# Kernel tuning notes

Measured on AMD Instinct MI355X. Metric: run time of the kernel, lower is better.

The kernel has to match this reference:

```python
import jax, jax.numpy as jnp
import numpy as np

N0, N1, N2 = 120000, 40000, 10000   # sampled node counts per hop
E0, E1 = 600000, 150000             # edges per block (fanout ~15)
DIN, DH, NC = 128, 256, 47


def _glorot(k, fan_in, fan_out):
    s = (2.0 / (fan_in + fan_out)) ** 0.5
    return jax.random.normal(k, (fan_in, fan_out), jnp.float32) * s


def setup_inputs() -> dict:
    key = jax.random.key(0)
    ks = jax.random.split(key, 20)
    x0 = jax.random.normal(ks[0], (N0, DIN), jnp.float32)
    src0 = jax.random.randint(ks[1], (E0,), 0, N0)
    dst0 = jax.random.randint(ks[2], (E0,), 0, N1)
    src1 = jax.random.randint(ks[3], (E1,), 0, N1)
    dst1 = jax.random.randint(ks[4], (E1,), 0, N2)
    srcb0 = jax.random.randint(ks[5], (E0,), 0, N0)
    dstb0 = jax.random.randint(ks[6], (E0,), 0, N1)
    srcb1 = jax.random.randint(ks[7], (E1,), 0, N1)
    dstb1 = jax.random.randint(ks[8], (E1,), 0, N2)
    # id_old_value_new: must satisfy idx[:n] < n for every truncation length n,
    # i.e. idx[k] in [0, k+1)
    rng = np.random.default_rng(0)
    idx = jnp.asarray((rng.random(N0) * (np.arange(N0) + 1)).astype(np.int64))
    mix_ratio = jnp.float32(0.5)
    Wl0 = _glorot(ks[9], DIN, DH); Wr0 = _glorot(ks[10], DIN, DH)
    b0 = jnp.zeros((DH,), jnp.float32)
    Wl1 = _glorot(ks[11], DH, DH); Wr1 = _glorot(ks[12], DH, DH)
    b1 = jnp.zeros((DH,), jnp.float32)
    Wlin = _glorot(ks[13], DH, NC)
    blin = jnp.zeros((NC,), jnp.float32)
    return dict(x0=x0, src0=src0, dst0=dst0, src1=src1, dst1=dst1,
                srcb0=srcb0, dstb0=dstb0, srcb1=srcb1, dstb1=dstb1,
                idx=idx, mix_ratio=mix_ratio,
                Wl0=Wl0, Wr0=Wr0, b0=b0, Wl1=Wl1, Wr1=Wr1, b1=b1,
                Wlin=Wlin, blin=blin)


def _sage(x_all, root_x, src, dst, n_root, Wl, Wr, b):
    # PyG-style SAGEConv, mean aggregation: lin_l(mean_j x_j) + lin_r(root)
    msgs = x_all[src]                                        # [E, D] gather
    s = jax.ops.segment_sum(msgs, dst, num_segments=n_root)  # [n_root, D]
    cnt = jax.ops.segment_sum(jnp.ones_like(dst, dtype=x_all.dtype), dst,
                              num_segments=n_root)
    mean = s / jnp.maximum(cnt, 1.0)[:, None]
    return mean @ Wl + root_x @ Wr + b


def reference(x0, src0, dst0, src1, dst1, srcb0, dstb0, srcb1, dstb1,
              idx, mix_ratio, Wl0, Wr0, b0, Wl1, Wr1, b1, Wlin, blin):
    blocks = [(src0, dst0, N1), (src1, dst1, N2)]
    blocks_b = [(srcb0, dstb0, N1), (srcb1, dstb1, N2)]
    params = [(Wl0, Wr0, b0), (Wl1, Wr1, b1)]
    m = mix_ratio

    # first branch (dropout omitted: inference mode)
    aggr_xs = [x0]
    for i in range(2):
        src, dst, n_root = blocks[i]
        Wl, Wr, b = params[i]
        root_x = aggr_xs[-1][:n_root]
        x = jax.nn.relu(_sage(aggr_xs[-1], root_x, src, dst, n_root, Wl, Wr, b))
        aggr_xs.append(x)

    # permuted branch via id_old_value_new gather
    aggr_xs_b = [x[idx[: x.shape[0]]] for x in aggr_xs]

    x_mix = aggr_xs[0] * m + aggr_xs_b[0] * (1.0 - m)
    for i in range(2):
        src, dst, n_root = blocks[i]
        srcb, dstb, n_root_b = blocks_b[i]
        Wl, Wr, b = params[i]
        x_new = jax.nn.relu(_sage(aggr_xs[i], x_mix[:n_root], src, dst,
                                  n_root, Wl, Wr, b))
        x_new_b = jax.nn.relu(_sage(aggr_xs_b[i], x_mix[:n_root_b], srcb, dstb,
                                    n_root_b, Wl, Wr, b))
        x_mix = x_new * m + x_new_b * (1.0 - m)

    logits = x_mix @ Wlin + blin
    return jax.nn.log_softmax(logits, axis=-1)
```

## Files before the change

### kernel.cpp

```cpp
#include <hip/hip_runtime.h>
#include <math.h>

#define N1C 40000
#define N2C 10000
#define DIN 128
#define DH  256
#define NC  47

#define TOTCNT (2 * N1C + 2 * N2C)
#define CAP 64
#define CURSTR 16

typedef __attribute__((ext_vector_type(8))) short v8s;
typedef __attribute__((ext_vector_type(4))) float v4f;
typedef __attribute__((ext_vector_type(2))) float v2f;

#if __has_builtin(__builtin_amdgcn_cvt_pk_f32_fp8)
#define HW_FP8 1
#endif

__device__ __forceinline__ unsigned short f2bf(float f) {
    unsigned int u = __float_as_uint(f);
    u += 0x7FFF + ((u >> 16) & 1);
    return (unsigned short)(u >> 16);
}
__device__ __forceinline__ float bf2f(unsigned int h) {
    return __uint_as_float(h << 16);
}

__device__ __forceinline__ unsigned char f2e4m3(float f) {
    unsigned int u = __float_as_uint(f);
    unsigned char s = (unsigned char)((u >> 24) & 0x80);
    float a = __uint_as_float(u & 0x7FFFFFFF);
    if (a > 448.0f) a = 448.0f;
    if (a < 0.015625f) {
        int k = (int)rintf(a * 512.0f);
        return s | (unsigned char)k;
    }
    unsigned int bits = __float_as_uint(a);
    int et = (int)(bits >> 23) - 127 + 7;
    unsigned int m32 = bits & 0x7FFFFF;
    unsigned int m3 = m32 >> 20;
    unsigned int rest = m32 & 0xFFFFF;
    if (rest > 0x80000 || (rest == 0x80000 && (m3 & 1))) m3++;
    if (m3 == 8) { m3 = 0; et++; }
    if (et > 15 || (et == 15 && m3 == 7)) return s | 0x7E;
    return s | (unsigned char)((et << 3) | m3);
}

__device__ __forceinline__ void dec4(unsigned int u, float& f0, float& f1,
                                     float& f2, float& f3) {
#ifdef HW_FP8
    v2f lo = __builtin_amdgcn_cvt_pk_f32_fp8((int)u, false);
    v2f hi = __builtin_amdgcn_cvt_pk_f32_fp8((int)u, true);
    f0 = lo[0]; f1 = lo[1]; f2 = hi[0]; f3 = hi[1];
#else
    auto d1 = [](unsigned int b) -> float {
        int e = (b >> 3) & 15, mm = b & 7;
        float d = (e == 0) ? (float)mm * (1.0f / 512.0f)
                           : (1.0f + (float)mm * 0.125f) * exp2f((float)(e - 7));
        return (b & 0x80) ? -d : d;
    };
    f0 = d1(u & 0xFF); f1 = d1((u >> 8) & 0xFF);
    f2 = d1((u >> 16) & 0xFF); f3 = d1(u >> 24);
#endif
}

__global__ __launch_bounds__(256) void front_fused(
        const int* __restrict__ src0, const int* __restrict__ dst0,
        const int* __restrict__ srcb0, const int* __restrict__ dstb0,
        const int* __restrict__ src1, const int* __restrict__ dst1,
        const int* __restrict__ srcb1, const int* __restrict__ dstb1,
        const int* __restrict__ perm, int* __restrict__ cur,
        int* __restrict__ bucket, int E0, int E1, int nbFill,
        const float* __restrict__ x0, unsigned char* __restrict__ x0f,
        long n8, int nbConv,
        const float* __restrict__ Wl0, const float* __restrict__ Wr0,
        const float* __restrict__ Wl1, const float* __restrict__ Wr1,
        unsigned short* __restrict__ Wt0l, unsigned short* __restrict__ Wt0r,
        unsigned short* __restrict__ Wt1l, unsigned short* __restrict__ Wt1r) {
    int b = blockIdx.x, t = threadIdx.x;
    if (b < nbFill) {
        int e = b * 256 + t;
        int tot = 2 * E0 + 2 * E1;
        if (e >= tot) return;
        int s, bin;
        if (e < E0) {
            s = src0[e];                  bin = dst0[e];
        } else if (e < 2 * E0) {
            int le = e - E0;
            s = perm[srcb0[le]];          bin = N1C + dstb0[le];
        } else if (e < 2 * E0 + E1) {
            int le = e - 2 * E0;
            s = src1[le];                 bin = 2 * N1C + dst1[le];
        } else {
            int le = e - 2 * E0 - E1;
            s = perm[srcb1[le]];          bin = 2 * N1C + N2C + dstb1[le];
        }
        int pos = atomicAdd(&cur[(size_t)bin * CURSTR], 1);
        if (pos < CAP) bucket[(size_t)bin * CAP + pos] = s;
    } else if (b < nbFill + nbConv) {
        long i = (long)(b - nbFill) * 256 + t;
        if (i >= n8) return;
        const float4* p = (const float4*)(x0 + i * 8);
        float4 a = p[0], c = p[1];
        float f[8] = {a.x, a.y, a.z, a.w, c.x, c.y, c.z, c.w};
        unsigned int q0 = 0, q1 = 0;
#pragma unroll
        for (int j = 0; j < 8; j++) {
            unsigned int e8 = f2e4m3(f[j]);
            if (j < 4) q0 |= e8 << (8 * j); else q1 |= e8 << (8 * (j - 4));
        }
        uint2 q = {q0, q1};
        *(uint2*)(x0f + i * 8) = q;
    } else {
        int id = (b - nbFill - nbConv) * 256 + t;
        const int S0 = DIN * DH;
        const int S1 = DH * DH;
        const float* W; unsigned short* Wt; int K, loc;
        if (id < S0)                   { W = Wl0; Wt = Wt0l; K = DIN; loc = id; }
        else if (id < 2 * S0)          { W = Wr0; Wt = Wt0r; K = DIN; loc = id - S0; }
        else if (id < 2 * S0 + S1)     { W = Wl1; Wt = Wt1l; K = DH;  loc = id - 2 * S0; }
        else if (id < 2 * S0 + 2 * S1) { W = Wr1; Wt = Wt1r; K = DH;  loc = id - 2 * S0 - S1; }
        else return;
        int n = loc / K, k = loc - n * K;
        Wt[(size_t)n * K + k] = f2bf(W[(size_t)k * DH + n]);
    }
}

__global__ __launch_bounds__(256) void gather_mean_128f(
        const unsigned char* __restrict__ xf, const int* __restrict__ bucket,
        const int* __restrict__ cur, unsigned short* __restrict__ mean0,
        unsigned short* __restrict__ meanb0) {
    const int half = N1C / 8;
    int b = blockIdx.x;
    int binbase; unsigned short* outp; int rb;
    if (b < half) { binbase = 0;   outp = mean0;  rb = b; }
    else          { binbase = N1C; outp = meanb0; rb = b - half; }
    int wv = threadIdx.x >> 6, lane = threadIdx.x & 63;
    int row = rb * 8 + wv * 2 + (lane >> 5);
    int c4 = (lane & 31) * 4;
    int bin = binbase + row;
    int cnt = min(cur[(size_t)bin * CURSTR], CAP);
    const int* cs = bucket + (size_t)bin * CAP;
    float a0 = 0.0f, a1 = 0.0f, a2 = 0.0f, a3 = 0.0f;
    int i = 0;
    for (; i + 3 < cnt; i += 4) {
        int s0 = cs[i], s1 = cs[i + 1], s2 = cs[i + 2], s3 = cs[i + 3];
        unsigned int u = *(const unsigned int*)&xf[(size_t)s0 * DIN + c4];
        unsigned int v = *(const unsigned int*)&xf[(size_t)s1 * DIN + c4];
        unsigned int w = *(const unsigned int*)&xf[(size_t)s2 * DIN + c4];
        unsigned int z = *(const unsigned int*)&xf[(size_t)s3 * DIN + c4];
        float u0, u1, u2, u3, w0, w1, w2, w3, p0, p1, p2, p3, q0, q1, q2, q3;
        dec4(u, u0, u1, u2, u3);
        dec4(v, w0, w1, w2, w3);
        dec4(w, p0, p1, p2, p3);
        dec4(z, q0, q1, q2, q3);
        a0 += (u0 + w0) + (p0 + q0); a1 += (u1 + w1) + (p1 + q1);
        a2 += (u2 + w2) + (p2 + q2); a3 += (u3 + w3) + (p3 + q3);
    }
    for (; i < cnt; i++) {
        unsigned int u = *(const unsigned int*)&xf[(size_t)cs[i] * DIN + c4];
        float u0, u1, u2, u3;
        dec4(u, u0, u1, u2, u3);
        a0 += u0; a1 += u1; a2 += u2; a3 += u3;
    }
    float inv = 1.0f / (float)max(cnt, 1);
    uint2 o;
    o.x = (unsigned int)f2bf(a0 * inv) | ((unsigned int)f2bf(a1 * inv) << 16);
    o.y = (unsigned int)f2bf(a2 * inv) | ((unsigned int)f2bf(a3 * inv) << 16);
    *(uint2*)&outp[(size_t)row * DIN + c4] = o;
}

__global__ __launch_bounds__(256) void gather_mean_256f(
        const unsigned char* __restrict__ xf, const int* __restrict__ bucket,
        const int* __restrict__ cur, unsigned short* __restrict__ mean1,
        unsigned short* __restrict__ meanb1) {
    const int half = N2C / 4;
    int b = blockIdx.x;
    int binbase; unsigned short* outp; int rb;
    if (b < half) { binbase = 2 * N1C;       outp = mean1;  rb = b; }
    else          { binbase = 2 * N1C + N2C; outp = meanb1; rb = b - half; }
    int row = rb * 4 + (threadIdx.x >> 6);
    int lane = threadIdx.x & 63;
    int bin = binbase + row;
    int cnt = min(cur[(size_t)bin * CURSTR], CAP);
    const int* cs = bucket + (size_t)bin * CAP;
    float a0 = 0.0f, a1 = 0.0f, a2 = 0.0f, a3 = 0.0f;
    int i = 0;
    for (; i + 3 < cnt; i += 4) {
        int s0 = cs[i], s1 = cs[i + 1], s2 = cs[i + 2], s3 = cs[i + 3];
        unsigned int u = *(const unsigned int*)&xf[(size_t)s0 * DH + lane * 4];
        unsigned int v = *(const unsigned int*)&xf[(size_t)s1 * DH + lane * 4];
        unsigned int w = *(const unsigned int*)&xf[(size_t)s2 * DH + lane * 4];
        unsigned int z = *(const unsigned int*)&xf[(size_t)s3 * DH + lane * 4];
        float u0, u1, u2, u3, w0, w1, w2, w3, p0, p1, p2, p3, q0, q1, q2, q3;
        dec4(u, u0, u1, u2, u3);
        dec4(v, w0, w1, w2, w3);
        dec4(w, p0, p1, p2, p3);
        dec4(z, q0, q1, q2, q3);
        a0 += (u0 + w0) + (p0 + q0); a1 += (u1 + w1) + (p1 + q1);
        a2 += (u2 + w2) + (p2 + q2); a3 += (u3 + w3) + (p3 + q3);
    }
    for (; i < cnt; i++) {
        unsigned int u = *(const unsigned int*)&xf[(size_t)cs[i] * DH + lane * 4];
        float u0, u1, u2, u3;
        dec4(u, u0, u1, u2, u3);
        a0 += u0; a1 += u1; a2 += u2; a3 += u3;
    }
    float inv = 1.0f / (float)max(cnt, 1);
    uint2 o;
    o.x = (unsigned int)f2bf(a0 * inv) | ((unsigned int)f2bf(a1 * inv) << 16);
    o.y = (unsigned int)f2bf(a2 * inv) | ((unsigned int)f2bf(a3 * inv) << 16);
    *(uint2*)&outp[(size_t)row * DH + lane * 4] = o;
}

#define KP0 136
#define H0T 5
__global__ __launch_bounds__(256, 2) void hop0_mfma(
        const float* __restrict__ x0, const int* __restrict__ idx,
        const unsigned short* __restrict__ mean0, const unsigned short* __restrict__ meanb0,
        const unsigned short* __restrict__ Wtl, const unsigned short* __restrict__ Wtr,
        const float* __restrict__ b, const float* __restrict__ mixp,
        unsigned char* __restrict__ x1f, unsigned short* __restrict__ xm1) {
    __shared__ unsigned short Alds[4][16][KP0];
    int t = threadIdx.x;
    int wv = t >> 6, lane = t & 63;
    int mrow = lane & 15, quad = lane >> 4;
    float m = *mixp;

    v8s wl[4][4], wr[4][4];
    float bb[4];
#pragma unroll
    for (int ct = 0; ct < 4; ct++) {
        int n = wv * 64 + mrow * 4 + ct;
        bb[ct] = b[n];
#pragma unroll
        for (int ks = 0; ks < 4; ks++) {
            int k0 = ks * 32 + quad * 8;
            wl[ct][ks] = *(const v8s*)&Wtl[(size_t)n * DIN + k0];
            wr[ct][ks] = *(const v8s*)&Wtr[(size_t)n * DIN + k0];
        }
    }

    for (int tile = 0; tile < H0T; tile++) {
        int row0 = (blockIdx.x * H0T + tile) * 16;
        {
            int r = t >> 4, k0 = (t & 15) * 8;
            int rg = row0 + r;
            *(v8s*)&Alds[0][r][k0] = *(const v8s*)&mean0[(size_t)rg * DIN + k0];
            *(v8s*)&Alds[1][r][k0] = *(const v8s*)&meanb0[(size_t)rg * DIN + k0];
            const float4* xr4 = (const float4*)&x0[(size_t)rg * DIN + k0];
            float4 A0 = xr4[0], A1 = xr4[1];
            int ib = idx[rg];
            const float4* xb4 = (const float4*)&x0[(size_t)ib * DIN + k0];
            float4 B0 = xb4[0], B1 = xb4[1];
            float fa[8] = {A0.x, A0.y, A0.z, A0.w, A1.x, A1.y, A1.z, A1.w};
            float fb[8] = {B0.x, B0.y, B0.z, B0.w, B1.x, B1.y, B1.z, B1.w};
            v8s vr, vm;
#pragma unroll
            for (int j = 0; j < 8; j++) {
                vr[j] = (short)f2bf(fa[j]);
                vm[j] = (short)f2bf(m * fa[j] + (1.0f - m) * fb[j]);
            }
            *(v8s*)&Alds[2][r][k0] = vr;
            *(v8s*)&Alds[3][r][k0] = vm;
        }
        __syncthreads();
        v4f accA[4], accB[4], accC[4], accD[4];
#pragma unroll
        for (int ct = 0; ct < 4; ct++) {
            accA[ct] = (v4f){0.f, 0.f, 0.f, 0.f}; accB[ct] = (v4f){0.f, 0.f, 0.f, 0.f};
            accC[ct] = (v4f){0.f, 0.f, 0.f, 0.f}; accD[ct] = (v4f){0.f, 0.f, 0.f, 0.f};
        }
#pragma unroll
        for (int ks = 0; ks < 4; ks++) {
            int k0 = ks * 32 + quad * 8;
            v8s aM = *(v8s*)&Alds[0][mrow][k0];
            v8s aB = *(v8s*)&Alds[1][mrow][k0];
            v8s aR = *(v8s*)&Alds[2][mrow][k0];
            v8s aX = *(v8s*)&Alds[3][mrow][k0];
#pragma unroll
            for (int ct = 0; ct < 4; ct++) {
                accA[ct] = __builtin_amdgcn_mfma_f32_16x16x32_bf16(aM, wl[ct][ks], accA[ct], 0, 0, 0);
                accB[ct] = __builtin_amdgcn_mfma_f32_16x16x32_bf16(aB, wl[ct][ks], accB[ct], 0, 0, 0);
                accC[ct] = __builtin_amdgcn_mfma_f32_16x16x32_bf16(aR, wr[ct][ks], accC[ct], 0, 0, 0);
                accD[ct] = __builtin_amdgcn_mfma_f32_16x16x32_bf16(aX, wr[ct][ks], accD[ct], 0, 0, 0);
            }
        }
        int colb = wv * 64 + mrow * 4;
#pragma unroll
        for (int r = 0; r < 4; r++) {
            int row = row0 + quad * 4 + r;
            unsigned int xpack = 0;
            unsigned int s01, s23;
            unsigned short sh[4];
#pragma unroll
            for (int ct = 0; ct < 4; ct++) {
                float pA = accA[ct][r], pB = accB[ct][r], pC = accC[ct][r], pD = accD[ct][r];
                float xv  = fmaxf(pA + pC + bb[ct], 0.0f);
                float xn  = fmaxf(pA + pD + bb[ct], 0.0f);
                float xnb = fmaxf(pB + pD + bb[ct], 0.0f);
                xpack |= ((unsigned int)f2e4m3(xv)) << (8 * ct);
                sh[ct] = f2bf(m * xn + (1.0f - m) * xnb);
            }
            s01 = (unsigned int)sh[0] | ((unsigned int)sh[1] << 16);
            s23 = (unsigned int)sh[2] | ((unsigned int)sh[3] << 16);
            *(unsigned int*)&x1f[(size_t)row * DH + colb] = xpack;
            uint2 xm = {s01, s23};
            *(uint2*)&xm1[(size_t)row * DH + colb] = xm;
        }
        __syncthreads();
    }
}

#define KP1 264
#define H1T 2
__global__ __launch_bounds__(256, 2) void hop1_mfma(
        const unsigned short* __restrict__ mean1, const unsigned short* __restrict__ meanb1,
        const unsigned short* __restrict__ xm1,
        const unsigned short* __restrict__ Wtl, const unsigned short* __restrict__ Wtr,
        const float* __restrict__ b, const float* __restrict__ mixp,
        float* __restrict__ xm2) {
    __shared__ unsigned short Alds[3][16][KP1];
    int t = threadIdx.x;
    int wv = t >> 6, lane = t & 63;
    int mrow = lane & 15, quad = lane >> 4;
    float m = *mixp;

    v8s wlc[4][4], wrc[4][4];
    float bb[4];
#pragma unroll
    for (int ct = 0; ct < 4; ct++) {
        int n = wv * 64 + mrow * 4 + ct;
        bb[ct] = b[n];
#pragma unroll
        for (int ks = 0; ks < 4; ks++) {
            int k0 = ks * 32 + quad * 8;
            wlc[ct][ks] = *(const v8s*)&Wtl[(size_t)n * DH + k0];
            wrc[ct][ks] = *(const v8s*)&Wtr[(size_t)n * DH + k0];
        }
    }

    for (int tt = 0; tt < H1T; tt++) {
        int tIdx = blockIdx.x * H1T + tt;
        if (tIdx >= N2C / 16) break;
        int row0 = tIdx * 16;
        {
            int r = t >> 4, k0 = (t & 15) * 16;
            int rg = row0 + r;
            *(v8s*)&Alds[0][r][k0]     = *(const v8s*)&mean1[(size_t)rg * DH + k0];
            *(v8s*)&Alds[0][r][k0 + 8] = *(const v8s*)&mean1[(size_t)rg * DH + k0 + 8];
            *(v8s*)&Alds[1][r][k0]     = *(const v8s*)&meanb1[(size_t)rg * DH + k0];
            *(v8s*)&Alds[1][r][k0 + 8] = *(const v8s*)&meanb1[(size_t)rg * DH + k0 + 8];
            *(v8s*)&Alds[2][r][k0]     = *(const v8s*)&xm1[(size_t)rg * DH + k0];
            *(v8s*)&Alds[2][r][k0 + 8] = *(const v8s*)&xm1[(size_t)rg * DH + k0 + 8];
        }
        __syncthreads();
        v4f accA[4], accB[4], accC[4];
#pragma unroll
        for (int ct = 0; ct < 4; ct++) {
            accA[ct] = (v4f){0.f, 0.f, 0.f, 0.f};
            accB[ct] = (v4f){0.f, 0.f, 0.f, 0.f};
            accC[ct] = (v4f){0.f, 0.f, 0.f, 0.f};
        }
#pragma unroll
        for (int ks = 0; ks < 8; ks++) {
            int k0 = ks * 32 + quad * 8;
            v8s aM = *(v8s*)&Alds[0][mrow][k0];
            v8s aB = *(v8s*)&Alds[1][mrow][k0];
            v8s aR = *(v8s*)&Alds[2][mrow][k0];
#pragma unroll
            for (int ct = 0; ct < 4; ct++) {
                v8s bl, br;
                if (ks < 4) { bl = wlc[ct][ks]; br = wrc[ct][ks]; }
                else {
                    int n = wv * 64 + mrow * 4 + ct;
                    bl = *(const v8s*)&Wtl[(size_t)n * DH + k0];
                    br = *(const v8s*)&Wtr[(size_t)n * DH + k0];
                }
                accA[ct] = __builtin_amdgcn_mfma_f32_16x16x32_bf16(aM, bl, accA[ct], 0, 0, 0);
                accB[ct] = __builtin_amdgcn_mfma_f32_16x16x32_bf16(aB, bl, accB[ct], 0, 0, 0);
                accC[ct] = __builtin_amdgcn_mfma_f32_16x16x32_bf16(aR, br, accC[ct], 0, 0, 0);
            }
        }
        int colb = wv * 64 + mrow * 4;
#pragma unroll
        for (int r = 0; r < 4; r++) {
            int row = row0 + quad * 4 + r;
            float4 o;
            float v0 = fmaxf(accA[0][r] + accC[0][r] + bb[0], 0.0f);
            float w0 = fmaxf(accB[0][r] + accC[0][r] + bb[0], 0.0f);
            float v1 = fmaxf(accA[1][r] + accC[1][r] + bb[1], 0.0f);
            float w1 = fmaxf(accB[1][r] + accC[1][r] + bb[1], 0.0f);
            float v2 = fmaxf(accA[2][r] + accC[2][r] + bb[2], 0.0f);
            float w2 = fmaxf(accB[2][r] + accC[2][r] + bb[2], 0.0f);
            float v3 = fmaxf(accA[3][r] + accC[3][r] + bb[3], 0.0f);
            float w3 = fmaxf(accB[3][r] + accC[3][r] + bb[3], 0.0f);
            o.x = m * v0 + (1.0f - m) * w0;
            o.y = m * v1 + (1.0f - m) * w1;
            o.z = m * v2 + (1.0f - m) * w2;
            o.w = m * v3 + (1.0f - m) * w3;
            *(float4*)&xm2[(size_t)row * DH + colb] = o;
        }
        __syncthreads();
    }
}

__global__ __launch_bounds__(256) void logits_lsm(
        const float* __restrict__ xmix2, const float* __restrict__ Wlin,
        const float* __restrict__ blin, float* __restrict__ out, int nrows) {
    int w = threadIdx.x >> 6;
    int row = blockIdx.x * 4 + w;
    if (row >= nrows) return;
    int t = threadIdx.x & 63;
    __shared__ float xs[4][DH];
    for (int i = t; i < DH; i += 64) xs[w][i] = xmix2[(size_t)row * DH + i];
    __builtin_amdgcn_s_waitcnt(0);
    float acc = 0.0f;
    if (t < NC) {
        acc = blin[t];
        for (int k = 0; k < DH; k++) acc += xs[w][k] * Wlin[k * NC + t];
    }
    float v = (t < NC) ? acc : -INFINITY;
    float mx = v;
    for (int off = 32; off; off >>= 1) mx = fmaxf(mx, __shfl_xor(mx, off, 64));
    float ex = (t < NC) ? expf(acc - mx) : 0.0f;
    float sum = ex;
    for (int off = 32; off; off >>= 1) sum += __shfl_xor(sum, off, 64);
    if (t < NC) out[(size_t)row * NC + t] = acc - mx - logf(sum);
}

extern "C" void kernel_launch(void* const* d_in, const int* in_sizes, int n_in,
                              void* d_out, int out_size, void* d_ws, size_t ws_size,
                              hipStream_t stream) {
    const float* x0    = (const float*)d_in[0];
    const int*   src0  = (const int*)d_in[1];
    const int*   dst0  = (const int*)d_in[2];
    const int*   src1  = (const int*)d_in[3];
    const int*   dst1  = (const int*)d_in[4];
    const int*   srcb0 = (const int*)d_in[5];
    const int*   dstb0 = (const int*)d_in[6];
    const int*   srcb1 = (const int*)d_in[7];
    const int*   dstb1 = (const int*)d_in[8];
    const int*   idx   = (const int*)d_in[9];
    const float* mixp  = (const float*)d_in[10];
    const float* Wl0   = (const float*)d_in[11];
    const float* Wr0   = (const float*)d_in[12];
    const float* b0    = (const float*)d_in[13];
    const float* Wl1   = (const float*)d_in[14];
    const float* Wr1   = (const float*)d_in[15];
    const float* b1    = (const float*)d_in[16];
    const float* Wlin  = (const float*)d_in[17];
    const float* blin  = (const float*)d_in[18];
    float* out = (float*)d_out;

    const int E0 = in_sizes[1];
    const int E1 = in_sizes[3];
    const long x0elems = (long)in_sizes[0];

    int* wsi    = (int*)d_ws;
    int* cur    = wsi;
    int* bucket = cur + (size_t)TOTCNT * CURSTR;
    unsigned short* wsh = (unsigned short*)(bucket + (size_t)TOTCNT * CAP);
    unsigned short* mean0  = wsh;
    unsigned short* meanb0 = mean0  + (size_t)N1C * DIN;
    unsigned short* mean1  = meanb0 + (size_t)N1C * DIN;
    unsigned short* meanb1 = mean1  + (size_t)N2C * DH;
    unsigned short* xm1h   = meanb1 + (size_t)N2C * DH;
    unsigned short* Wt0l   = xm1h   + (size_t)N1C * DH;
    unsigned short* Wt0r   = Wt0l + DIN * DH;
    unsigned short* Wt1l   = Wt0r + DIN * DH;
    unsigned short* Wt1r   = Wt1l + DH * DH;
    float* xm2 = (float*)(Wt1r + DH * DH);
    unsigned char* x0f = (unsigned char*)(xm2 + (size_t)N2C * DH);
    unsigned char* x1f = x0f + (size_t)x0elems;

    hipMemsetAsync(cur, 0, sizeof(int) * (size_t)TOTCNT * CURSTR, stream);

    int etot = 2 * E0 + 2 * E1;
    int nbFill = (etot + 255) / 256;
    long n8 = x0elems / 8;
    int nbConv = (int)((n8 + 255) / 256);
    int nbW = (2 * DIN * DH + 2 * DH * DH + 255) / 256;
    front_fused<<<nbFill + nbConv + nbW, 256, 0, stream>>>(
        src0, dst0, srcb0, dstb0, src1, dst1, srcb1, dstb1, idx, cur, bucket,
        E0, E1, nbFill, x0, x0f, n8, nbConv,
        Wl0, Wr0, Wl1, Wr1, Wt0l, Wt0r, Wt1l, Wt1r);

    gather_mean_128f<<<2 * (N1C / 8), 256, 0, stream>>>(x0f, bucket, cur, mean0, meanb0);

    hop0_mfma<<<N1C / (16 * H0T), 256, 0, stream>>>(x0, idx, mean0, meanb0, Wt0l, Wt0r,
                                                    b0, mixp, x1f, xm1h);

    gather_mean_256f<<<2 * (N2C / 4), 256, 0, stream>>>(x1f, bucket, cur, mean1, meanb1);

    hop1_mfma<<<(N2C / 16 + H1T - 1) / H1T, 256, 0, stream>>>(mean1, meanb1, xm1h,
                                                              Wt1l, Wt1r, b1, mixp, xm2);

    logits_lsm<<<(N2C + 3) / 4, 256, 0, stream>>>(xm2, Wlin, blin, out, N2C);
}
```

Before: 341.1 us.

## Fuse logits/log-softmax into hop1 and widen gather loads to 8 bytes

The final linear layer and log-softmax move into the hop1 MFMA kernel. The mixed hop1 output is staged in shared memory, so the fp32 xm2 buffer is no longer written to and re-read from global memory, and one launch is removed. Separately, both gather-mean kernels now load 8 fp8 values per lane per neighbor instead of 4 and store 16-byte results, which halves the number of threads per row. The trade-off is that the logits stage now runs on only 313 hop1 blocks with a serial 256-step dot product per wave, so it gets much less parallelism than the standalone kernel had.

```diff
diff --git a/kernel.cpp b/kernel.cpp
--- a/kernel.cpp
+++ b/kernel.cpp
@@ -26,6 +26,9 @@
 }
 __device__ __forceinline__ float bf2f(unsigned int h) {
     return __uint_as_float(h << 16);
+}
+__device__ __forceinline__ unsigned int packbf(float a, float b) {
+    return (unsigned int)f2bf(a) | ((unsigned int)f2bf(b) << 16);
 }
 
 __device__ __forceinline__ unsigned char f2e4m3(float f) {
@@ -64,6 +67,11 @@
     f0 = d1(u & 0xFF); f1 = d1((u >> 8) & 0xFF);
     f2 = d1((u >> 16) & 0xFF); f3 = d1(u >> 24);
 #endif
+}
+__device__ __forceinline__ void acc8(uint2 u, float* a) {
+    float f0, f1, f2, f3;
+    dec4(u.x, f0, f1, f2, f3); a[0] += f0; a[1] += f1; a[2] += f2; a[3] += f3;
+    dec4(u.y, f0, f1, f2, f3); a[4] += f0; a[5] += f1; a[6] += f2; a[7] += f3;
 }
 
 __global__ __launch_bounds__(256) void front_fused(
@@ -132,87 +140,74 @@
         const unsigned char* __restrict__ xf, const int* __restrict__ bucket,
         const int* __restrict__ cur, unsigned short* __restrict__ mean0,
         unsigned short* __restrict__ meanb0) {
-    const int half = N1C / 8;
+    const int half = N1C / 16;
     int b = blockIdx.x;
     int binbase; unsigned short* outp; int rb;
     if (b < half) { binbase = 0;   outp = mean0;  rb = b; }
     else          { binbase = N1C; outp = meanb0; rb = b - half; }
     int wv = threadIdx.x >> 6, lane = threadIdx.x & 63;
-    int row = rb * 8 + wv * 2 + (lane >> 5);
-    int c4 = (lane & 31) * 4;
+    int row = rb * 16 + wv * 4 + (lane >> 4);
+    int c8 = (lane & 15) * 8;
     int bin = binbase + row;
     int cnt = min(cur[(size_t)bin * CURSTR], CAP);
     const int* cs = bucket + (size_t)bin * CAP;
-    float a0 = 0.0f, a1 = 0.0f, a2 = 0.0f, a3 = 0.0f;
+    float a[8] = {0, 0, 0, 0, 0, 0, 0, 0};
     int i = 0;
-    for (; i + 3 < cnt; i += 4) {
-        int s0 = cs[i], s1 = cs[i + 1], s2 = cs[i + 2], s3 = cs[i + 3];
-        unsigned int u = *(const unsigned int*)&xf[(size_t)s0 * DIN + c4];
-        unsigned int v = *(const unsigned int*)&xf[(size_t)s1 * DIN + c4];
-        unsigned int w = *(const unsigned int*)&xf[(size_t)s2 * DIN + c4];
-        unsigned int z = *(const unsigned int*)&xf[(size_t)s3 * DIN + c4];
-        float u0, u1, u2, u3, w0, w1, w2, w3, p0, p1, p2, p3, q0, q1, q2, q3;
-        dec4(u, u0, u1, u2, u3);
-        dec4(v, w0, w1, w2, w3);
-        dec4(w, p0, p1, p2, p3);
-        dec4(z, q0, q1, q2, q3);
-        a0 += (u0 + w0) + (p0 + q0); a1 += (u1 + w1) + (p1 + q1);
-        a2 += (u2 + w2) + (p2 + q2); a3 += (u3 + w3) + (p3 + q3);
-    }
-    for (; i < cnt; i++) {
-        unsigned int u = *(const unsigned int*)&xf[(size_t)cs[i] * DIN + c4];
-        float u0, u1, u2, u3;
-        dec4(u, u0, u1, u2, u3);
-        a0 += u0; a1 += u1; a2 += u2; a3 += u3;
+    for (; i + 1 < cnt; i += 2) {
+        int s0 = cs[i], s1 = cs[i + 1];
+        uint2 u = *(const uint2*)&xf[(size_t)s0 * DIN + c8];
+        uint2 v = *(const uint2*)&xf[(size_t)s1 * DIN + c8];
+        acc8(u, a);
+        acc8(v, a);
+    }
+    if (i < cnt) {
+        uint2 u = *(const uint2*)&xf[(size_t)cs[i] * DIN + c8];
+        acc8(u, a);
     }
     float inv = 1.0f / (float)max(cnt, 1);
-    uint2 o;
-    o.x = (unsigned int)f2bf(a0 * inv) | ((unsigned int)f2bf(a1 * inv) << 16);
-    o.y = (unsigned int)f2bf(a2 * inv) | ((unsigned int)f2bf(a3 * inv) << 16);
-    *(uint2*)&outp[(size_t)row * DIN + c4] = o;
+    uint4 o;
+    o.x = packbf(a[0] * inv, a[1] * inv);
+    o.y = packbf(a[2] * inv, a[3] * inv);
+    o.z = packbf(a[4] * inv, a[5] * inv);
+    o.w = packbf(a[6] * inv, a[7] * inv);
+    *(uint4*)&outp[(size_t)row * DIN + c8] = o;
 }
 
 __global__ __launch_bounds__(256) void gather_mean_256f(
         const unsigned char* __restrict__ xf, const int* __restrict__ bucket,
         const int* __restrict__ cur, unsigned short* __restrict__ mean1,
         unsigned short* __restrict__ meanb1) {
-    const int half = N2C / 4;
+    const int half = N2C / 8;
     int b = blockIdx.x;
     int binbase; unsigned short* outp; int rb;
     if (b < half) { binbase = 2 * N1C;       outp = mean1;  rb = b; }
     else          { binbase = 2 * N1C + N2C; outp = meanb1; rb = b - half; }
-    int row = rb * 4 + (threadIdx.x >> 6);
-    int lane = threadIdx.x & 63;
+    int wv = threadIdx.x >> 6, lane = threadIdx.x & 63;
+    int row = rb * 8 + wv * 2 + (lane >> 5);
+    int c8 = (lane & 31) * 8;
     int bin = binbase + row;
     int cnt = min(cur[(size_t)bin * CURSTR], CAP);
     const int* cs = bucket + (size_t)bin * CAP;
-    float a0 = 0.0f, a1 = 0.0f, a2 = 0.0f, a3 = 0.0f;
+    float a[8] = {0, 0, 0, 0, 0, 0, 0, 0};
     int i = 0;
-    for (; i + 3 < cnt; i += 4) {
-        int s0 = cs[i], s1 = cs[i + 1], s2 = cs[i + 2], s3 = cs[i + 3];
-        unsigned int u = *(const unsigned int*)&xf[(size_t)s0 * DH + lane * 4];
-        unsigned int v = *(const unsigned int*)&xf[(size_t)s1 * DH + lane * 4];
-        unsigned int w = *(const unsigned int*)&xf[(size_t)s2 * DH + lane * 4];
-        unsigned int z = *(const unsigned int*)&xf[(size_t)s3 * DH + lane * 4];
-        float u0, u1, u2, u3, w0, w1, w2, w3, p0, p1, p2, p3, q0, q1, q2, q3;
-        dec4(u, u0, u1, u2, u3);
-        dec4(v, w0, w1, w2, w3);
-        dec4(w, p0, p1, p2, p3);
-        dec4(z, q0, q1, q2, q3);
-        a0 += (u0 + w0) + (p0 + q0); a1 += (u1 + w1) + (p1 + q1);
-        a2 += (u2 + w2) + (p2 + q2); a3 += (u3 + w3) + (p3 + q3);
-    }
-    for (; i < cnt; i++) {
-        unsigned int u = *(const unsigned int*)&xf[(size_t)cs[i] * DH + lane * 4];
-        float u0, u1, u2, u3;
-        dec4(u, u0, u1, u2, u3);
-        a0 += u0; a1 += u1; a2 += u2; a3 += u3;
+    for (; i + 1 < cnt; i += 2) {
+        int s0 = cs[i], s1 = cs[i + 1];
+        uint2 u = *(const uint2*)&xf[(size_t)s0 * DH + c8];
+        uint2 v = *(const uint2*)&xf[(size_t)s1 * DH + c8];
+        acc8(u, a);
+        acc8(v, a);
+    }
+    if (i < cnt) {
+        uint2 u = *(const uint2*)&xf[(size_t)cs[i] * DH + c8];
+        acc8(u, a);
     }
     float inv = 1.0f / (float)max(cnt, 1);
-    uint2 o;
-    o.x = (unsigned int)f2bf(a0 * inv) | ((unsigned int)f2bf(a1 * inv) << 16);
-    o.y = (unsigned int)f2bf(a2 * inv) | ((unsigned int)f2bf(a3 * inv) << 16);
-    *(uint2*)&outp[(size_t)row * DH + lane * 4] = o;
+    uint4 o;
+    o.x = packbf(a[0] * inv, a[1] * inv);
+    o.y = packbf(a[2] * inv, a[3] * inv);
+    o.z = packbf(a[4] * inv, a[5] * inv);
+    o.w = packbf(a[6] * inv, a[7] * inv);
+    *(uint4*)&outp[(size_t)row * DH + c8] = o;
 }
 
 #define KP0 136
@@ -293,7 +288,6 @@
         for (int r = 0; r < 4; r++) {
             int row = row0 + quad * 4 + r;
             unsigned int xpack = 0;
-            unsigned int s01, s23;
             unsigned short sh[4];
 #pragma unroll
             for (int ct = 0; ct < 4; ct++) {
@@ -304,10 +298,9 @@
                 xpack |= ((unsigned int)f2e4m3(xv)) << (8 * ct);
                 sh[ct] = f2bf(m * xn + (1.0f - m) * xnb);
             }
-            s01 = (unsigned int)sh[0] | ((unsigned int)sh[1] << 16);
-            s23 = (unsigned int)sh[2] | ((unsigned int)sh[3] << 16);
             *(unsigned int*)&x1f[(size_t)row * DH + colb] = xpack;
-            uint2 xm = {s01, s23};
+            uint2 xm = {(unsigned int)sh[0] | ((unsigned int)sh[1] << 16),
+                        (unsigned int)sh[2] | ((unsigned int)sh[3] << 16)};
             *(uint2*)&xm1[(size_t)row * DH + colb] = xm;
         }
         __syncthreads();
@@ -316,13 +309,15 @@
 
 #define KP1 264
 #define H1T 2
-__global__ __launch_bounds__(256, 2) void hop1_mfma(
+__global__ __launch_bounds__(256, 2) void hop1_fused(
         const unsigned short* __restrict__ mean1, const unsigned short* __restrict__ meanb1,
         const unsigned short* __restrict__ xm1,
         const unsigned short* __restrict__ Wtl, const unsigned short* __restrict__ Wtr,
         const float* __restrict__ b, const float* __restrict__ mixp,
-        float* __restrict__ xm2) {
+        const float* __restrict__ Wlin, const float* __restrict__ blin,
+        float* __restrict__ out) {
     __shared__ unsigned short Alds[3][16][KP1];
+    __shared__ float xs[16][DH];
     int t = threadIdx.x;
     int wv = t >> 6, lane = t & 63;
     int mrow = lane & 15, quad = lane >> 4;
@@ -387,7 +382,7 @@
         int colb = wv * 64 + mrow * 4;
 #pragma unroll
         for (int r = 0; r < 4; r++) {
-            int row = row0 + quad * 4 + r;
+            int lr = quad * 4 + r;
             float4 o;
             float v0 = fmaxf(accA[0][r] + accC[0][r] + bb[0], 0.0f);
             float w0 = fmaxf(accB[0][r] + accC[0][r] + bb[0], 0.0f);
@@ -401,34 +396,28 @@
             o.y = m * v1 + (1.0f - m) * w1;
             o.z = m * v2 + (1.0f - m) * w2;
             o.w = m * v3 + (1.0f - m) * w3;
-            *(float4*)&xm2[(size_t)row * DH + colb] = o;
+            *(float4*)&xs[lr][colb] = o;
         }
         __syncthreads();
-    }
-}
-
-__global__ __launch_bounds__(256) void logits_lsm(
-        const float* __restrict__ xmix2, const float* __restrict__ Wlin,
-        const float* __restrict__ blin, float* __restrict__ out, int nrows) {
-    int w = threadIdx.x >> 6;
-    int row = blockIdx.x * 4 + w;
-    if (row >= nrows) return;
-    int t = threadIdx.x & 63;
-    __shared__ float xs[4][DH];
-    for (int i = t; i < DH; i += 64) xs[w][i] = xmix2[(size_t)row * DH + i];
-    __builtin_amdgcn_s_waitcnt(0);
-    float acc = 0.0f;
-    if (t < NC) {
-        acc = blin[t];
-        for (int k = 0; k < DH; k++) acc += xs[w][k] * Wlin[k * NC + t];
-    }
-    float v = (t < NC) ? acc : -INFINITY;
-    float mx = v;
-    for (int off = 32; off; off >>= 1) mx = fmaxf(mx, __shfl_xor(mx, off, 64));
-    float ex = (t < NC) ? expf(acc - mx) : 0.0f;
-    float sum = ex;
-    for (int off = 32; off; off >>= 1) sum += __shfl_xor(sum, off, 64);
-    if (t < NC) out[(size_t)row * NC + t] = acc - mx - logf(sum);
+#pragma unroll
+        for (int rr = 0; rr < 4; rr++) {
+            int lr = wv * 4 + rr;
+            int grow = row0 + lr;
+            float acc = 0.0f;
+            if (lane < NC) {
+                acc = blin[lane];
+                for (int k = 0; k < DH; k++) acc += xs[lr][k] * Wlin[k * NC + lane];
+            }
+            float v = (lane < NC) ? acc : -INFINITY;
+            float mx = v;
+            for (int off = 32; off; off >>= 1) mx = fmaxf(mx, __shfl_xor(mx, off, 64));
+            float ex = (lane < NC) ? expf(acc - mx) : 0.0f;
+            float sum = ex;
+            for (int off = 32; off; off >>= 1) sum += __shfl_xor(sum, off, 64);
+            if (lane < NC) out[(size_t)grow * NC + lane] = acc - mx - logf(sum);
+        }
+        __syncthreads();
+    }
 }
 
 extern "C" void kernel_launch(void* const* d_in, const int* in_sizes, int n_in,
@@ -472,8 +461,7 @@
     unsigned short* Wt0r   = Wt0l + DIN * DH;
     unsigned short* Wt1l   = Wt0r + DIN * DH;
     unsigned short* Wt1r   = Wt1l + DH * DH;
-    float* xm2 = (float*)(Wt1r + DH * DH);
-    unsigned char* x0f = (unsigned char*)(xm2 + (size_t)N2C * DH);
+    unsigned char* x0f = (unsigned char*)(Wt1r + DH * DH);
     unsigned char* x1f = x0f + (size_t)x0elems;
 
     hipMemsetAsync(cur, 0, sizeof(int) * (size_t)TOTCNT * CURSTR, stream);
@@ -488,15 +476,13 @@
         E0, E1, nbFill, x0, x0f, n8, nbConv,
         Wl0, Wr0, Wl1, Wr1, Wt0l, Wt0r, Wt1l, Wt1r);
 
-    gather_mean_128f<<<2 * (N1C / 8), 256, 0, stream>>>(x0f, bucket, cur, mean0, meanb0);
+    gather_mean_128f<<<2 * (N1C / 16), 256, 0, stream>>>(x0f, bucket, cur, mean0, meanb0);
 
     hop0_mfma<<<N1C / (16 * H0T), 256, 0, stream>>>(x0, idx, mean0, meanb0, Wt0l, Wt0r,
                                                     b0, mixp, x1f, xm1h);
 
-    gather_mean_256f<<<2 * (N2C / 4), 256, 0, stream>>>(x1f, bucket, cur, mean1, meanb1);
-
-    hop1_mfma<<<(N2C / 16 + H1T - 1) / H1T, 256, 0, stream>>>(mean1, meanb1, xm1h,
-                                                              Wt1l, Wt1r, b1, mixp, xm2);
-
-    logits_lsm<<<(N2C + 3) / 4, 256, 0, stream>>>(xm2, Wlin, blin, out, N2C);
-}
+    gather_mean_256f<<<2 * (N2C / 8), 256, 0, stream>>>(x1f, bucket, cur, mean1, meanb1);
+
+    hop1_fused<<<(N2C / 16 + H1T - 1) / H1T, 256, 0, stream>>>(
+        mean1, meanb1, xm1h, Wt1l, Wt1r, b1, mixp, Wlin, blin, out);
+}
```

Result: slower. 358.1 us (+5.0%).
